# Kernel tuning notes

Measured on AMD Instinct MI355X. Metric: run time of the kernel, lower is better.

## Reference

```python
import jax, jax.numpy as jnp
import numpy as np

DIM = 1024
B, S = 2, 2048

def _gelu(v):
    return jax.nn.gelu(v, approximate=False)

def setup_inputs() -> dict:
    key = jax.random.key(0)
    ks = jax.random.split(key, 24)
    d = DIM
    def lin(k, fan_in, fan_out):
        k1, k2 = jax.random.split(k)
        bound = 1.0 / np.sqrt(fan_in)
        W = jax.random.uniform(k1, (fan_in, fan_out), jnp.float32, -bound, bound)
        b = jax.random.uniform(k2, (fan_out,), jnp.float32, -bound, bound)
        return W, b
    w_pt1, b_pt1 = lin(ks[0], d, 2 * d)
    w_pt2, b_pt2 = lin(ks[1], 2 * d, d)
    w_wg, b_wg = lin(ks[2], d, d)
    w_mag, b_mag = lin(ks[3], d, d)
    w_q1, b_q1 = lin(ks[4], d, d)
    w_q2, b_q2 = lin(ks[5], d, d)
    w_mix, b_mix = lin(ks[6], d, 2 * d)
    w_o1, b_o1 = lin(ks[7], d, d)
    w_o2, b_o2 = lin(ks[8], d, d)
    return {
        "x": jax.random.normal(ks[9], (B, S, d), jnp.float32),
        "w_pt1": w_pt1, "b_pt1": b_pt1, "w_pt2": w_pt2, "b_pt2": b_pt2,
        "int_scale": jnp.ones((d,), jnp.float32) * 0.001,
        "w_wg": w_wg, "b_wg": b_wg,
        "gate_temp": jnp.ones((1,), jnp.float32) * 2.0,
        "w_mag": w_mag, "b_mag": b_mag,
        "w_q1": w_q1, "b_q1": b_q1, "w_q2": w_q2, "b_q2": b_q2,
        "w_mix": w_mix, "b_mix": b_mix,
        "ln_g": jnp.ones((d,), jnp.float32), "ln_b": jnp.zeros((d,), jnp.float32),
        "w_o1": w_o1, "b_o1": b_o1, "w_o2": w_o2, "b_o2": b_o2,
    }

def reference(x, w_pt1, b_pt1, w_pt2, b_pt2, int_scale, w_wg, b_wg, gate_temp,
              w_mag, b_mag, w_q1, b_q1, w_q2, b_q2, w_mix, b_mix,
              ln_g, ln_b, w_o1, b_o1, w_o2, b_o2):
    # input-dependent phase basis
    phase_delta = _gelu(x @ w_pt1 + b_pt1) @ w_pt2 + b_pt2          # [B,S,D]
    phi = jnp.cumsum(phase_delta * jnp.abs(int_scale), axis=1)
    # selective write gate + magnitude
    write_gate = jax.nn.sigmoid((x @ w_wg + b_wg) * gate_temp)
    magnitude = jax.nn.sigmoid(x @ w_mag + b_mag) * 5.0
    content = write_gate * x * magnitude
    # complex-phase memory accumulation (4 seq-length scans)
    memory_real = jnp.cumsum(content * jnp.cos(phi), axis=1)
    memory_imag = jnp.cumsum(content * jnp.sin(phi), axis=1)
    accum_weight = jnp.cumsum(write_gate * magnitude + 1e-8, axis=1)
    inv_s = 1.0 / jnp.sqrt(accum_weight)
    mr, mi = memory_real * inv_s, memory_imag * inv_s
    # query-phase retrieval (complex rotation)
    query_phase = phi + (_gelu(x @ w_q1 + b_q1) @ w_q2 + b_q2)
    cq, sq = jnp.cos(query_phase), jnp.sin(query_phase)
    retrieved_real = mr * cq + mi * sq
    retrieved_imag = mi * cq - mr * sq
    # input-dependent output mixing
    mix = x @ w_mix + b_mix
    d = x.shape[-1]
    mix_real = jax.nn.sigmoid(mix[..., :d])
    mix_imag = jax.nn.sigmoid(mix[..., d:])
    retrieved = mix_real * retrieved_real + mix_imag * retrieved_imag
    # output head: LayerNorm -> Linear -> GELU -> (Dropout=identity in eval) -> Linear
    mu = jnp.mean(retrieved, axis=-1, keepdims=True)
    var = jnp.var(retrieved, axis=-1, keepdims=True)
    ln = (retrieved - mu) / jnp.sqrt(var + 1e-5) * ln_g + ln_b
    out = _gelu(ln @ w_o1 + b_o1) @ w_o2 + b_o2
    return x + out
```

## Files before the change

### kernel.cpp

```cpp
#include <hip/hip_runtime.h>
#include <hip/hip_bf16.h>

#define MTOT 4096
#define DD   1024
#define D2   2048
#define SS   2048
#define BB   2
#define NC2  64
#define CL2  (SS/NC2)

typedef __attribute__((ext_vector_type(8))) short bf16x8;
typedef __attribute__((ext_vector_type(4))) float f32x4;

__device__ __forceinline__ float sigmf(float v){
    return 1.0f/(1.0f+__expf(-v));
}
__device__ __forceinline__ float geluf(float v){
    float u = 0.7978845608f*v*(1.0f + 0.044715f*v*v);
    float e = __expf(2.0f*u);
    float t = 1.0f - 2.0f/(e + 1.0f);
    return 0.5f*v*(1.0f + t);
}
__device__ __forceinline__ ushort f2bf(float f){
    unsigned u = __float_as_uint(f);
    unsigned r = (u + 0x7FFF + ((u>>16)&1)) >> 16;
    return (ushort)r;
}
__device__ __forceinline__ float bf2f(ushort u){
    return __uint_as_float(((unsigned)u)<<16);
}

__device__ __forceinline__ void stage_tile(
    const ushort* __restrict__ A, const ushort* __restrict__ Bt, int K,
    int m0, int n0, int k0, ushort* As, ushort* Bs)
{
    int tid = threadIdx.x;
    #pragma unroll
    for (int i = 0; i < 2; i++) {
        int e = (i*256 + tid) * 8;
        int r = e >> 5;
        int s = (e >> 3) & 3;
        int c = ((s ^ ((r >> 1) & 3)) << 3);
        __builtin_amdgcn_global_load_lds(
            (const __attribute__((address_space(1))) void*)(A + (size_t)(m0 + r)*K + k0 + c),
            (__attribute__((address_space(3))) void*)(As + e), 16, 0, 0);
        __builtin_amdgcn_global_load_lds(
            (const __attribute__((address_space(1))) void*)(Bt + (size_t)(n0 + r)*K + k0 + c),
            (__attribute__((address_space(3))) void*)(Bs + e), 16, 0, 0);
    }
}

__device__ __forceinline__ void load_frags(
    const ushort* As, const ushort* Bs, int wr, int wc, int lrow, int cs,
    bf16x8 (&af)[4], bf16x8 (&bfr)[4])
{
    #pragma unroll
    for (int i = 0; i < 4; i++) {
        int ra = wr*64 + i*16 + lrow;
        int rb = wc*64 + i*16 + lrow;
        af[i]  = *(const bf16x8*)(As + ra*32 + ((cs ^ ((ra>>1)&3))<<3));
        bfr[i] = *(const bf16x8*)(Bs + rb*32 + ((cs ^ ((rb>>1)&3))<<3));
    }
}

__device__ __forceinline__ void do_mfma(
    const bf16x8 (&af)[4], const bf16x8 (&bfr)[4], f32x4 (&acc)[4][4])
{
    __builtin_amdgcn_s_setprio(1);
    #pragma unroll
    for (int i = 0; i < 4; i++)
        #pragma unroll
        for (int j = 0; j < 4; j++)
            acc[i][j] = __builtin_amdgcn_mfma_f32_16x16x32_bf16(af[i], bfr[j], acc[i][j], 0, 0, 0);
    __builtin_amdgcn_s_setprio(0);
}

__device__ __forceinline__ void mgemm_core(
    const ushort* __restrict__ A, const ushort* __restrict__ Bt, int K,
    int m0, int n0, ushort (&As)[2][4096], ushort (&Bs)[2][4096], f32x4 (&acc)[4][4])
{
    int lane = threadIdx.x & 63, wave = threadIdx.x >> 6;
    int wr = wave >> 1, wc = wave & 1;
    int lrow = lane & 15, cs = lane >> 4;
    int NT = K >> 5;
    stage_tile(A, Bt, K, m0, n0, 0,  As[0], Bs[0]);
    stage_tile(A, Bt, K, m0, n0, 32, As[1], Bs[1]);
    for (int t = 0; t < NT-1; ++t) {
        asm volatile("s_waitcnt vmcnt(4)" ::: "memory");
        __builtin_amdgcn_s_barrier();
        bf16x8 af[4], bfr[4];
        load_frags(As[t&1], Bs[t&1], wr, wc, lrow, cs, af, bfr);
        if (t < NT-2) {
            asm volatile("s_waitcnt lgkmcnt(0)" ::: "memory");
            __builtin_amdgcn_s_barrier();
            stage_tile(A, Bt, K, m0, n0, (t+2) << 5, As[t&1], Bs[t&1]);
        }
        __builtin_amdgcn_sched_barrier(0);
        do_mfma(af, bfr, acc);
    }
    asm volatile("s_waitcnt vmcnt(0)" ::: "memory");
    __builtin_amdgcn_s_barrier();
    bf16x8 af[4], bfr[4];
    load_frags(As[(NT-1)&1], Bs[(NT-1)&1], wr, wc, lrow, cs, af, bfr);
    do_mfma(af, bfr, acc);
}

__global__ __launch_bounds__(256,4) void mgemmA_k(
    const ushort* __restrict__ xb, const ushort* __restrict__ Wt,
    const float* __restrict__ b_pt1, const float* __restrict__ b_wg,
    const float* __restrict__ b_mag, const float* __restrict__ b_q1,
    const float* __restrict__ b_mix, const float* __restrict__ gtemp,
    ushort* __restrict__ H1b, ushort* __restrict__ wgb, ushort* __restrict__ magb,
    ushort* __restrict__ Hqb, ushort* __restrict__ mixb)
{
    __shared__ ushort As[2][4096], Bs[2][4096];
    int bid = blockIdx.x;
    int xcd = bid & 7, local = bid >> 3;
    int m0 = (xcd*4 + (local & 3)) * 128;
    int n0 = (local >> 2) * 128;
    f32x4 acc[4][4] = {};
    mgemm_core(xb, Wt, 1024, m0, n0, As, Bs, acc);
    int lane = threadIdx.x & 63, wave = threadIdx.x >> 6;
    int wr = wave >> 1, wc = wave & 1;
    int rng = n0 >> 10;
    float gt = gtemp[0];
    #pragma unroll
    for (int i = 0; i < 4; i++) {
        int mb = m0 + wr*64 + i*16 + (lane>>4)*4;
        #pragma unroll
        for (int j = 0; j < 4; j++) {
            int n = n0 + wc*64 + j*16 + (lane&15);
            #pragma unroll
            for (int r = 0; r < 4; r++) {
                int m = mb + r;
                float v = acc[i][j][r];
                if (rng < 2) {
                    H1b[(size_t)m*D2 + n] = f2bf(geluf(v + b_pt1[n]));
                } else if (rng == 2) {
                    wgb[(size_t)m*DD + n-2048] = f2bf(sigmf((v + b_wg[n-2048])*gt));
                } else if (rng == 3) {
                    magb[(size_t)m*DD + n-3072] = f2bf(sigmf(v + b_mag[n-3072])*5.0f);
                } else if (rng == 4) {
                    Hqb[(size_t)m*DD + n-4096] = f2bf(geluf(v + b_q1[n-4096]));
                } else {
                    mixb[(size_t)m*D2 + n-5120] = f2bf(sigmf(v + b_mix[n-5120]));
                }
            }
        }
    }
}

__global__ __launch_bounds__(256,4) void mgemmBC_k(
    const ushort* __restrict__ H1b, const ushort* __restrict__ wt_pt2,
    const ushort* __restrict__ Hqb, const ushort* __restrict__ wt_q2,
    const float* __restrict__ b_pt2, const float* __restrict__ b_q2,
    const float* __restrict__ iscale,
    ushort* __restrict__ pdb, ushort* __restrict__ qadjb)
{
    __shared__ ushort As[2][4096], Bs[2][4096];
    int bid = blockIdx.x;
    int xcd = bid & 7, local = bid >> 3;
    int m0 = (xcd*4 + (local & 3)) * 128;
    int rest = local >> 2;
    int z = rest >> 3;
    int n0 = (rest & 7) * 128;
    const ushort* A  = z ? Hqb   : H1b;
    const ushort* Bt = z ? wt_q2 : wt_pt2;
    const float* bias = z ? b_q2 : b_pt2;
    int K = z ? 1024 : 2048;
    ushort* outp = z ? qadjb : pdb;
    f32x4 acc[4][4] = {};
    mgemm_core(A, Bt, K, m0, n0, As, Bs, acc);
    int lane = threadIdx.x & 63, wave = threadIdx.x >> 6;
    int wr = wave >> 1, wc = wave & 1;
    #pragma unroll
    for (int i = 0; i < 4; i++) {
        int mb = m0 + wr*64 + i*16 + (lane>>4)*4;
        #pragma unroll
        for (int j = 0; j < 4; j++) {
            int n = n0 + wc*64 + j*16 + (lane&15);
            float bv = bias[n];
            float sc = z ? 1.0f : fabsf(iscale[n]);
            #pragma unroll
            for (int r = 0; r < 4; r++) {
                float v = acc[i][j][r] + bv;
                outp[(size_t)(mb+r)*DD + n] = f2bf(z ? v : v*sc);
            }
        }
    }
}

template<int ACT, bool RESID, bool OUTBF16>
__global__ __launch_bounds__(256,4) void mgemm_k(
    const ushort* __restrict__ A, const ushort* __restrict__ Bt,
    const float* __restrict__ bias, const float* __restrict__ resid,
    void* __restrict__ Cout, int N, int K)
{
    __shared__ ushort As[2][4096], Bs[2][4096];
    int bid = blockIdx.x;
    int xcd = bid & 7, local = bid >> 3;
    int m0 = (xcd*4 + (local & 3)) * 128;
    int n0 = (local >> 2) * 128;
    f32x4 acc[4][4] = {};
    mgemm_core(A, Bt, K, m0, n0, As, Bs, acc);
    int lane = threadIdx.x & 63, wave = threadIdx.x >> 6;
    int wr = wave >> 1, wc = wave & 1;
    #pragma unroll
    for (int i = 0; i < 4; i++) {
        int mb = m0 + wr*64 + i*16 + (lane>>4)*4;
        #pragma unroll
        for (int j = 0; j < 4; j++) {
            int n = n0 + wc*64 + j*16 + (lane&15);
            float bv = bias[n];
            #pragma unroll
            for (int r = 0; r < 4; r++) {
                size_t idx = (size_t)(mb + r)*N + n;
                float v = acc[i][j][r] + bv;
                if (ACT==1) v = geluf(v);
                if (RESID) v += resid[idx];
                if (OUTBF16) ((ushort*)Cout)[idx] = f2bf(v);
                else         ((float*)Cout)[idx]  = v;
            }
        }
    }
}

__global__ __launch_bounds__(256) void cvt_bf16_k(const float* __restrict__ in, ushort* __restrict__ outp){
    size_t i = ((size_t)blockIdx.x*256 + threadIdx.x)*8;
    float4 a = *(const float4*)(in + i);
    float4 b = *(const float4*)(in + i + 4);
    ushort t[8];
    t[0]=f2bf(a.x); t[1]=f2bf(a.y); t[2]=f2bf(a.z); t[3]=f2bf(a.w);
    t[4]=f2bf(b.x); t[5]=f2bf(b.y); t[6]=f2bf(b.z); t[7]=f2bf(b.w);
    *(int4*)(outp + i) = *(const int4*)t;
}

__device__ __forceinline__ void tcvt_body(const float* W, ushort* Wt, int K, int N){
    __shared__ float tile[32][33];
    int n0 = blockIdx.x*32, k0 = blockIdx.y*32;
    int tx = threadIdx.x & 7, ty = threadIdx.x >> 3;
    float4 v = *(const float4*)(W + (size_t)(k0+ty)*N + n0 + tx*4);
    tile[ty][tx*4+0]=v.x; tile[ty][tx*4+1]=v.y; tile[ty][tx*4+2]=v.z; tile[ty][tx*4+3]=v.w;
    __syncthreads();
    ushort t[4];
    #pragma unroll
    for (int i=0;i<4;i++) t[i] = f2bf(tile[tx*4+i][ty]);
    *(uint2*)(Wt + (size_t)(n0+ty)*K + k0 + tx*4) = *(const uint2*)t;
}

__global__ __launch_bounds__(256) void tcvt_k(const float* __restrict__ W, ushort* __restrict__ Wt, int K, int N){
    tcvt_body(W, Wt, K, N);
}
__global__ __launch_bounds__(256) void tcvt2_k(const float* __restrict__ w0, ushort* __restrict__ o0,
                                               const float* __restrict__ w1, ushort* __restrict__ o1){
    tcvt_body(blockIdx.z ? w1 : w0, blockIdx.z ? o1 : o0, 1024, 2048);
}
__global__ __launch_bounds__(256) void tcvt6_k(
    const float* __restrict__ w0, ushort* __restrict__ o0,
    const float* __restrict__ w1, ushort* __restrict__ o1,
    const float* __restrict__ w2, ushort* __restrict__ o2,
    const float* __restrict__ w3, ushort* __restrict__ o3,
    const float* __restrict__ w4, ushort* __restrict__ o4,
    const float* __restrict__ w5, ushort* __restrict__ o5)
{
    const float* W; ushort* Wt;
    switch(blockIdx.z){
        case 0: W=w0; Wt=o0; break;
        case 1: W=w1; Wt=o1; break;
        case 2: W=w2; Wt=o2; break;
        case 3: W=w3; Wt=o3; break;
        case 4: W=w4; Wt=o4; break;
        default: W=w5; Wt=o5; break;
    }
    tcvt_body(W, Wt, 1024, 1024);
}

__global__ __launch_bounds__(256) void passA_k(
    const ushort* __restrict__ pdb, float* __restrict__ csum)
{
    int d0 = (blockIdx.x*256 + threadIdx.x)*2;
    int c = blockIdx.y, b = blockIdx.z;
    const ushort* p = pdb + ((size_t)b*SS + (size_t)c*CL2)*DD + d0;
    float s0 = 0.f, s1 = 0.f;
    for (int i = 0; i < CL2; i++){
        ushort2 v = *(const ushort2*)(p + (size_t)i*DD);
        s0 += bf2f(v.x); s1 += bf2f(v.y);
    }
    *(float2*)(csum + ((size_t)b*NC2 + c)*DD + d0) = make_float2(s0, s1);
}

__global__ void scan2_k(float* __restrict__ csum, int nchains){
    int idx = blockIdx.x*256 + threadIdx.x;
    if (idx >= nchains) return;
    int xg = idx / DD, d = idx % DD;
    float* p = csum + (size_t)xg*NC2*DD + d;
    float run = 0.f;
    for (int c = 0; c < NC2; c++){ float t = p[(size_t)c*DD]; p[(size_t)c*DD] = run; run += t; }
}

__global__ __launch_bounds__(256) void passB_k(
    const ushort* __restrict__ pdb, const ushort* __restrict__ wgb,
    const ushort* __restrict__ magb, const ushort* __restrict__ xb,
    const float* __restrict__ csum_phi, float* __restrict__ csum_tri)
{
    int d0 = (blockIdx.x*256 + threadIdx.x)*2;
    int c = blockIdx.y, b = blockIdx.z;
    size_t off = ((size_t)b*SS + (size_t)c*CL2)*DD + d0;
    float2 phv = *(const float2*)(csum_phi + ((size_t)b*NC2 + c)*DD + d0);
    float ph0 = phv.x, ph1 = phv.y;
    float a0=0.f, a1=0.f, b0=0.f, b1=0.f, c0=0.f, c1=0.f;
    for (int i = 0; i < CL2; i++){
        size_t o = off + (size_t)i*DD;
        ushort2 pdv = *(const ushort2*)(pdb + o);
        ushort2 wgv = *(const ushort2*)(wgb + o);
        ushort2 mgv = *(const ushort2*)(magb + o);
        ushort2 xv  = *(const ushort2*)(xb + o);
        ph0 += bf2f(pdv.x); ph1 += bf2f(pdv.y);
        float w0 = bf2f(wgv.x), w1 = bf2f(wgv.y);
        float m0 = bf2f(mgv.x), m1 = bf2f(mgv.y);
        float ct0 = w0*bf2f(xv.x)*m0, ct1 = w1*bf2f(xv.y)*m1;
        float sp0, cp0, sp1, cp1;
        sincosf(ph0, &sp0, &cp0); sincosf(ph1, &sp1, &cp1);
        a0 += ct0*cp0; a1 += ct1*cp1;
        b0 += ct0*sp0; b1 += ct1*sp1;
        c0 += fmaf(w0, m0, 1e-8f); c1 += fmaf(w1, m1, 1e-8f);
    }
    size_t cs = ((size_t)b*NC2 + c)*DD + d0;
    size_t G = (size_t)BB*NC2*DD;
    *(float2*)(csum_tri + cs)     = make_float2(a0, a1);
    *(float2*)(csum_tri + G+cs)   = make_float2(b0, b1);
    *(float2*)(csum_tri + 2*G+cs) = make_float2(c0, c1);
}

__global__ __launch_bounds__(256) void passC_k(
    const ushort* __restrict__ pdb, const ushort* __restrict__ wgb,
    const ushort* __restrict__ magb, const ushort* __restrict__ xb,
    const ushort* __restrict__ qadjb, const ushort* __restrict__ mixb,
    const float* __restrict__ csum_phi, const float* __restrict__ csum_tri,
    ushort* __restrict__ ret)
{
    int d0 = (blockIdx.x*256 + threadIdx.x)*2;
    int c = blockIdx.y, b = blockIdx.z;
    size_t off = ((size_t)b*SS + (size_t)c*CL2)*DD + d0;
    size_t cs = ((size_t)b*NC2 + c)*DD + d0;
    size_t G = (size_t)BB*NC2*DD;
    float2 phv = *(const float2*)(csum_phi + cs);
    float2 r0v = *(const float2*)(csum_tri + cs);
    float2 r1v = *(const float2*)(csum_tri + G+cs);
    float2 r2v = *(const float2*)(csum_tri + 2*G+cs);
    float ph0 = phv.x, ph1 = phv.y;
    float p0 = r0v.x, p1 = r0v.y, q0 = r1v.x, q1 = r1v.y, s0 = r2v.x, s1 = r2v.y;
    size_t row0 = (size_t)b*SS + (size_t)c*CL2;
    for (int i = 0; i < CL2; i++){
        size_t o = off + (size_t)i*DD;
        ushort2 pdv = *(const ushort2*)(pdb + o);
        ushort2 wgv = *(const ushort2*)(wgb + o);
        ushort2 mgv = *(const ushort2*)(magb + o);
        ushort2 xv  = *(const ushort2*)(xb + o);
        ushort2 qav = *(const ushort2*)(qadjb + o);
        size_t mb2 = (row0 + i)*D2 + d0;
        ushort2 mrv = *(const ushort2*)(mixb + mb2);
        ushort2 miv = *(const ushort2*)(mixb + mb2 + DD);
        ph0 += bf2f(pdv.x); ph1 += bf2f(pdv.y);
        float w0 = bf2f(wgv.x), w1 = bf2f(wgv.y);
        float m0 = bf2f(mgv.x), m1 = bf2f(mgv.y);
        float ct0 = w0*bf2f(xv.x)*m0, ct1 = w1*bf2f(xv.y)*m1;
        float sp0, cp0, sp1, cp1;
        sincosf(ph0, &sp0, &cp0); sincosf(ph1, &sp1, &cp1);
        p0 += ct0*cp0; p1 += ct1*cp1;
        q0 += ct0*sp0; q1 += ct1*sp1;
        s0 += fmaf(w0, m0, 1e-8f); s1 += fmaf(w1, m1, 1e-8f);
        float inv0 = rsqrtf(s0), inv1 = rsqrtf(s1);
        float mr0 = p0*inv0, mi0 = q0*inv0;
        float mr1 = p1*inv1, mi1 = q1*inv1;
        float sq0, cq0, sq1, cq1;
        sincosf(ph0 + bf2f(qav.x), &sq0, &cq0);
        sincosf(ph1 + bf2f(qav.y), &sq1, &cq1);
        float rr0 = mr0*cq0 + mi0*sq0, ri0 = mi0*cq0 - mr0*sq0;
        float rr1 = mr1*cq1 + mi1*sq1, ri1 = mi1*cq1 - mr1*sq1;
        ushort2 rv;
        rv.x = f2bf(bf2f(mrv.x)*rr0 + bf2f(miv.x)*ri0);
        rv.y = f2bf(bf2f(mrv.y)*rr1 + bf2f(miv.y)*ri1);
        *(ushort2*)(ret + o) = rv;
    }
}

__global__ __launch_bounds__(256) void ln_k(
    const ushort* __restrict__ ret, const float* __restrict__ ln_g,
    const float* __restrict__ ln_b, ushort* __restrict__ outp)
{
    int row = blockIdx.x;
    size_t base = (size_t)row*DD;
    int d0 = threadIdx.x*4;
    ushort4 rv = *(const ushort4*)(ret + base + d0);
    float v0 = bf2f(rv.x), v1 = bf2f(rv.y), v2 = bf2f(rv.z), v3 = bf2f(rv.w);
    float sum = v0+v1+v2+v3;
    float sumsq = v0*v0 + v1*v1 + v2*v2 + v3*v3;
    #pragma unroll
    for (int off=32; off; off>>=1){
        sum   += __shfl_down(sum,off);
        sumsq += __shfl_down(sumsq,off);
    }
    __shared__ float red[8];
    int lane = threadIdx.x & 63, wid = threadIdx.x >> 6;
    if (lane==0){ red[wid]=sum; red[4+wid]=sumsq; }
    __syncthreads();
    sum   = red[0]+red[1]+red[2]+red[3];
    sumsq = red[4]+red[5]+red[6]+red[7];
    float mu  = sum * (1.0f/DD);
    float var = sumsq*(1.0f/DD) - mu*mu;
    float rstd = rsqrtf(var + 1e-5f);
    float4 g = *(const float4*)(ln_g + d0);
    float4 bb = *(const float4*)(ln_b + d0);
    ushort4 ov;
    ov.x = f2bf((v0-mu)*rstd*g.x + bb.x);
    ov.y = f2bf((v1-mu)*rstd*g.y + bb.y);
    ov.z = f2bf((v2-mu)*rstd*g.z + bb.z);
    ov.w = f2bf((v3-mu)*rstd*g.w + bb.w);
    *(ushort4*)(outp + base + d0) = ov;
}

extern "C" void kernel_launch(void* const* d_in, const int* in_sizes, int n_in,
                              void* d_out, int out_size, void* d_ws, size_t ws_size,
                              hipStream_t stream)
{
    const float* x     = (const float*)d_in[0];
    const float* w_pt1 = (const float*)d_in[1];
    const float* b_pt1 = (const float*)d_in[2];
    const float* w_pt2 = (const float*)d_in[3];
    const float* b_pt2 = (const float*)d_in[4];
    const float* iscale= (const float*)d_in[5];
    const float* w_wg  = (const float*)d_in[6];
    const float* b_wg  = (const float*)d_in[7];
    const float* gtemp = (const float*)d_in[8];
    const float* w_mag = (const float*)d_in[9];
    const float* b_mag = (const float*)d_in[10];
    const float* w_q1  = (const float*)d_in[11];
    const float* b_q1  = (const float*)d_in[12];
    const float* w_q2  = (const float*)d_in[13];
    const float* b_q2  = (const float*)d_in[14];
    const float* w_mix = (const float*)d_in[15];
    const float* b_mix = (const float*)d_in[16];
    const float* ln_g  = (const float*)d_in[17];
    const float* ln_b  = (const float*)d_in[18];
    const float* w_o1  = (const float*)d_in[19];
    const float* b_o1  = (const float*)d_in[20];
    const float* w_o2  = (const float*)d_in[21];
    const float* b_o2  = (const float*)d_in[22];
    float* out = (float*)d_out;

    const size_t SZ = (size_t)MTOT*DD;
    ushort* u = (ushort*)d_ws;
    ushort* xb    = u;                 u += SZ;
    ushort* H1b   = u;                 u += 2*SZ;
    ushort* ret   = H1b;
    ushort* Hqb   = u;                 u += SZ;
    ushort* lnb   = Hqb;
    ushort* wgb   = u;                 u += SZ;
    ushort* magb  = u;                 u += SZ;
    ushort* mixb  = u;                 u += 2*SZ;
    ushort* Hob   = u;                 u += SZ;
    ushort* pdb   = u;                 u += SZ;
    ushort* qadjb = u;                 u += SZ;
    ushort* Wt_all= u;                 u += (size_t)7168*1024;
    ushort* wt_pt2= u;                 u += (size_t)1024*2048;
    ushort* wt_q2 = u;                 u += (size_t)1024*1024;
    ushort* wt_o1 = u;                 u += (size_t)1024*1024;
    ushort* wt_o2 = u;                 u += (size_t)1024*1024;
    float* csum_phi = (float*)u;
    float* csum_tri = csum_phi + (size_t)BB*NC2*DD;

    dim3 blk(256);
    cvt_bf16_k<<<dim3(SZ/2048), blk, 0, stream>>>(x, xb);
    tcvt2_k<<<dim3(64, 32, 2), blk, 0, stream>>>(w_pt1, Wt_all, w_mix, Wt_all + (size_t)5120*1024);
    tcvt6_k<<<dim3(32, 32, 6), blk, 0, stream>>>(
        w_wg,  Wt_all + (size_t)2048*1024,
        w_mag, Wt_all + (size_t)3072*1024,
        w_q1,  Wt_all + (size_t)4096*1024,
        w_q2,  wt_q2,  w_o1, wt_o1,  w_o2, wt_o2);
    tcvt_k<<<dim3(32, 64), blk, 0, stream>>>(w_pt2, wt_pt2, 2048, 1024);
    mgemmA_k<<<dim3(1792), blk, 0, stream>>>(xb, Wt_all, b_pt1, b_wg, b_mag, b_q1, b_mix,
                                             gtemp, H1b, wgb, magb, Hqb, mixb);
    mgemmBC_k<<<dim3(512), blk, 0, stream>>>(H1b, wt_pt2, Hqb, wt_q2, b_pt2, b_q2,
                                             iscale, pdb, qadjb);
    passA_k<<<dim3(DD/512, NC2, BB), blk, 0, stream>>>(pdb, csum_phi);
    scan2_k<<<dim3((BB*DD+255)/256), blk, 0, stream>>>(csum_phi, BB*DD);
    passB_k<<<dim3(DD/512, NC2, BB), blk, 0, stream>>>(pdb, wgb, magb, xb, csum_phi, csum_tri);
    scan2_k<<<dim3((3*BB*DD+255)/256), blk, 0, stream>>>(csum_tri, 3*BB*DD);
    passC_k<<<dim3(DD/512, NC2, BB), blk, 0, stream>>>(pdb, wgb, magb, xb, qadjb, mixb,
                                                       csum_phi, csum_tri, ret);
    ln_k<<<dim3(MTOT), blk, 0, stream>>>(ret, ln_g, ln_b, lnb);
    mgemm_k<1,false,true><<<dim3(256), blk, 0, stream>>>(lnb, wt_o1, b_o1, nullptr, Hob, DD, DD);
    mgemm_k<0,true,false><<<dim3(256), blk, 0, stream>>>(Hob, wt_o2, b_o2, x, out, DD, DD);
}
```

Baseline: 253.6 us.

## Fuse phase chunk sums into GEMM epilogue and merge weight transposes

The phase-delta GEMM epilogue now reduces each 16-row group with lane shuffles and writes per-chunk column sums directly, which removes the separate passA pass over pdb. Supporting this requires doubling the chunk count to 128 chunks of 16 rows, which doubles the block count of passB and passC and lengthens the serial scan2 chains. The three weight transpose-convert launches are also merged into a single launch. The csum_phi buffer doubles in size, so its allocation must already fit or memory could be overrun.

```diff
diff --git a/kernel.cpp b/kernel.cpp
--- a/kernel.cpp
+++ b/kernel.cpp
@@ -6,7 +6,7 @@
 #define D2   2048
 #define SS   2048
 #define BB   2
-#define NC2  64
+#define NC2  128
 #define CL2  (SS/NC2)
 
 typedef __attribute__((ext_vector_type(8))) short bf16x8;
@@ -155,7 +155,8 @@
     const ushort* __restrict__ Hqb, const ushort* __restrict__ wt_q2,
     const float* __restrict__ b_pt2, const float* __restrict__ b_q2,
     const float* __restrict__ iscale,
-    ushort* __restrict__ pdb, ushort* __restrict__ qadjb)
+    ushort* __restrict__ pdb, ushort* __restrict__ qadjb,
+    float* __restrict__ csum_phi)
 {
     __shared__ ushort As[2][4096], Bs[2][4096];
     int bid = blockIdx.x;
@@ -173,6 +174,7 @@
     mgemm_core(A, Bt, K, m0, n0, As, Bs, acc);
     int lane = threadIdx.x & 63, wave = threadIdx.x >> 6;
     int wr = wave >> 1, wc = wave & 1;
+    float csum_ij[4][4];
     #pragma unroll
     for (int i = 0; i < 4; i++) {
         int mb = m0 + wr*64 + i*16 + (lane>>4)*4;
@@ -181,10 +183,32 @@
             int n = n0 + wc*64 + j*16 + (lane&15);
             float bv = bias[n];
             float sc = z ? 1.0f : fabsf(iscale[n]);
+            float s = 0.f;
             #pragma unroll
             for (int r = 0; r < 4; r++) {
                 float v = acc[i][j][r] + bv;
-                outp[(size_t)(mb+r)*DD + n] = f2bf(z ? v : v*sc);
+                ushort bfv = f2bf(z ? v : v*sc);
+                outp[(size_t)(mb+r)*DD + n] = bfv;
+                s += bf2f(bfv);
+            }
+            csum_ij[i][j] = s;
+        }
+    }
+    if (z == 0) {
+        int b = m0 >> 11;
+        int c0 = (m0 & 2047) >> 4;
+        #pragma unroll
+        for (int i = 0; i < 4; i++) {
+            int c = c0 + wr*4 + i;
+            #pragma unroll
+            for (int j = 0; j < 4; j++) {
+                float s = csum_ij[i][j];
+                s += __shfl_xor(s, 16);
+                s += __shfl_xor(s, 32);
+                if ((lane >> 4) == 0) {
+                    int n = n0 + wc*64 + j*16 + (lane&15);
+                    csum_phi[((size_t)b*NC2 + c)*DD + n] = s;
+                }
             }
         }
     }
@@ -235,9 +259,8 @@
     *(int4*)(outp + i) = *(const int4*)t;
 }
 
-__device__ __forceinline__ void tcvt_body(const float* W, ushort* Wt, int K, int N){
+__device__ __forceinline__ void tcvt_body(const float* W, ushort* Wt, int K, int N, int n0, int k0){
     __shared__ float tile[32][33];
-    int n0 = blockIdx.x*32, k0 = blockIdx.y*32;
     int tx = threadIdx.x & 7, ty = threadIdx.x >> 3;
     float4 v = *(const float4*)(W + (size_t)(k0+ty)*N + n0 + tx*4);
     tile[ty][tx*4+0]=v.x; tile[ty][tx*4+1]=v.y; tile[ty][tx*4+2]=v.z; tile[ty][tx*4+3]=v.w;
@@ -248,45 +271,30 @@
     *(uint2*)(Wt + (size_t)(n0+ty)*K + k0 + tx*4) = *(const uint2*)t;
 }
 
-__global__ __launch_bounds__(256) void tcvt_k(const float* __restrict__ W, ushort* __restrict__ Wt, int K, int N){
-    tcvt_body(W, Wt, K, N);
-}
-__global__ __launch_bounds__(256) void tcvt2_k(const float* __restrict__ w0, ushort* __restrict__ o0,
-                                               const float* __restrict__ w1, ushort* __restrict__ o1){
-    tcvt_body(blockIdx.z ? w1 : w0, blockIdx.z ? o1 : o0, 1024, 2048);
-}
-__global__ __launch_bounds__(256) void tcvt6_k(
-    const float* __restrict__ w0, ushort* __restrict__ o0,
-    const float* __restrict__ w1, ushort* __restrict__ o1,
-    const float* __restrict__ w2, ushort* __restrict__ o2,
-    const float* __restrict__ w3, ushort* __restrict__ o3,
-    const float* __restrict__ w4, ushort* __restrict__ o4,
-    const float* __restrict__ w5, ushort* __restrict__ o5)
-{
-    const float* W; ushort* Wt;
-    switch(blockIdx.z){
-        case 0: W=w0; Wt=o0; break;
-        case 1: W=w1; Wt=o1; break;
-        case 2: W=w2; Wt=o2; break;
-        case 3: W=w3; Wt=o3; break;
-        case 4: W=w4; Wt=o4; break;
-        default: W=w5; Wt=o5; break;
-    }
-    tcvt_body(W, Wt, 1024, 1024);
-}
-
-__global__ __launch_bounds__(256) void passA_k(
-    const ushort* __restrict__ pdb, float* __restrict__ csum)
-{
-    int d0 = (blockIdx.x*256 + threadIdx.x)*2;
-    int c = blockIdx.y, b = blockIdx.z;
-    const ushort* p = pdb + ((size_t)b*SS + (size_t)c*CL2)*DD + d0;
-    float s0 = 0.f, s1 = 0.f;
-    for (int i = 0; i < CL2; i++){
-        ushort2 v = *(const ushort2*)(p + (size_t)i*DD);
-        s0 += bf2f(v.x); s1 += bf2f(v.y);
-    }
-    *(float2*)(csum + ((size_t)b*NC2 + c)*DD + d0) = make_float2(s0, s1);
+__global__ __launch_bounds__(256) void tcvt_all_k(
+    const float* __restrict__ w_pt1, const float* __restrict__ w_mix,
+    const float* __restrict__ w_wg,  const float* __restrict__ w_mag,
+    const float* __restrict__ w_q1,  const float* __restrict__ w_q2,
+    const float* __restrict__ w_o1,  const float* __restrict__ w_o2,
+    const float* __restrict__ w_pt2,
+    ushort* __restrict__ Wt_all, ushort* __restrict__ wt_q2,
+    ushort* __restrict__ wt_o1,  ushort* __restrict__ wt_o2,
+    ushort* __restrict__ wt_pt2)
+{
+    int bid = blockIdx.x;
+    const float* W; ushort* Wt; int K, N, tile;
+    if (bid < 2048)        { W=w_pt1; Wt=Wt_all;                      K=1024; N=2048; tile=bid; }
+    else if (bid < 4096)   { W=w_mix; Wt=Wt_all+(size_t)5120*1024;    K=1024; N=2048; tile=bid-2048; }
+    else if (bid < 5120)   { W=w_wg;  Wt=Wt_all+(size_t)2048*1024;    K=1024; N=1024; tile=bid-4096; }
+    else if (bid < 6144)   { W=w_mag; Wt=Wt_all+(size_t)3072*1024;    K=1024; N=1024; tile=bid-5120; }
+    else if (bid < 7168)   { W=w_q1;  Wt=Wt_all+(size_t)4096*1024;    K=1024; N=1024; tile=bid-6144; }
+    else if (bid < 8192)   { W=w_q2;  Wt=wt_q2;                       K=1024; N=1024; tile=bid-7168; }
+    else if (bid < 9216)   { W=w_o1;  Wt=wt_o1;                       K=1024; N=1024; tile=bid-8192; }
+    else if (bid < 10240)  { W=w_o2;  Wt=wt_o2;                       K=1024; N=1024; tile=bid-9216; }
+    else                   { W=w_pt2; Wt=wt_pt2;                      K=2048; N=1024; tile=bid-10240; }
+    int nx = N >> 5;
+    int n0 = (tile % nx) * 32, k0 = (tile / nx) * 32;
+    tcvt_body(W, Wt, K, N, n0, k0);
 }
 
 __global__ void scan2_k(float* __restrict__ csum, int nchains){
@@ -472,18 +480,13 @@
 
     dim3 blk(256);
     cvt_bf16_k<<<dim3(SZ/2048), blk, 0, stream>>>(x, xb);
-    tcvt2_k<<<dim3(64, 32, 2), blk, 0, stream>>>(w_pt1, Wt_all, w_mix, Wt_all + (size_t)5120*1024);
-    tcvt6_k<<<dim3(32, 32, 6), blk, 0, stream>>>(
-        w_wg,  Wt_all + (size_t)2048*1024,
-        w_mag, Wt_all + (size_t)3072*1024,
-        w_q1,  Wt_all + (size_t)4096*1024,
-        w_q2,  wt_q2,  w_o1, wt_o1,  w_o2, wt_o2);
-    tcvt_k<<<dim3(32, 64), blk, 0, stream>>>(w_pt2, wt_pt2, 2048, 1024);
+    tcvt_all_k<<<dim3(12288), blk, 0, stream>>>(w_pt1, w_mix, w_wg, w_mag, w_q1, w_q2,
+                                                w_o1, w_o2, w_pt2,
+                                                Wt_all, wt_q2, wt_o1, wt_o2, wt_pt2);
     mgemmA_k<<<dim3(1792), blk, 0, stream>>>(xb, Wt_all, b_pt1, b_wg, b_mag, b_q1, b_mix,
                                              gtemp, H1b, wgb, magb, Hqb, mixb);
     mgemmBC_k<<<dim3(512), blk, 0, stream>>>(H1b, wt_pt2, Hqb, wt_q2, b_pt2, b_q2,
-                                             iscale, pdb, qadjb);
-    passA_k<<<dim3(DD/512, NC2, BB), blk, 0, stream>>>(pdb, csum_phi);
+                                             iscale, pdb, qadjb, csum_phi);
     scan2_k<<<dim3((BB*DD+255)/256), blk, 0, stream>>>(csum_phi, BB*DD);
     passB_k<<<dim3(DD/512, NC2, BB), blk, 0, stream>>>(pdb, wgb, magb, xb, csum_phi, csum_tri);
     scan2_k<<<dim3((3*BB*DD+255)/256), blk, 0, stream>>>(csum_tri, 3*BB*DD);
```

Result: faster. 240.0 us (-5.3%).
